# Kernel optimization log

Hardware: AMD Instinct MI355X
Metric: run time of the kernel (lower is better)

The kernel has to match this reference:

```python
import jax, jax.numpy as jnp
import numpy as np
import math

N, D, E, M, MODS = 16384, 1024, 5, 64, 5
K = 1  # top-k for sparse router


def setup_inputs() -> dict:
    key = jax.random.key(0)
    ks = jax.random.split(key, 24)
    rn = lambda k, shape, s=1.0: jax.random.normal(k, shape, dtype=jnp.float32) * s
    inp = {
        'x': rn(ks[0], (N, D)),
        'spectrogram': rn(ks[1], (N, D)),
        'waveform': rn(ks[2], (N, D)),
        'pitch': rn(ks[3], (N, D)),
        'envelope': rn(ks[4], (N, D)),
        'phase': rn(ks[5], (N, D)),
        # routers (torch Linear: y = x @ W.T + b, W is [out,in]); init std=0.01
        'Wsoft': rn(ks[6], (E, D), 0.01), 'bsoft': jnp.zeros((E,), jnp.float32),
        'Wsparse': rn(ks[7], (E, D), 0.01), 'bsparse': jnp.zeros((E,), jnp.float32),
        # memory (plain randn, not re-initialized)
        'm_key': rn(ks[8], (M, D)), 'm_val': rn(ks[9], (M, E)),
        # experts: Linear(D,D) -> SiLU -> Linear(D,D), stacked over E
        'W1': rn(ks[10], (E, D, D), 0.01), 'b1': jnp.zeros((E, D), jnp.float32),
        'W2': rn(ks[11], (E, D, D), 0.01), 'b2': jnp.zeros((E, D), jnp.float32),
        # fusion gates: Linear(D,1) + sigmoid, one per modality
        'Wg': rn(ks[12], (MODS, D), 0.01), 'bg': jnp.zeros((MODS,), jnp.float32),
        # fusion projection: Linear(D*MODS, D)
        'Wf': rn(ks[13], (D, D * MODS), 0.01), 'bf': jnp.zeros((D,), jnp.float32),
    }
    return inp


def reference(x, spectrogram, waveform, pitch, envelope, phase,
              Wsoft, bsoft, Wsparse, bsparse, m_key, m_val,
              W1, b1, W2, b2, Wg, bg, Wf, bf):
    alpha_moe = jnp.float32(0.5)
    alpha_fusion = jnp.float32(0.5)

    # soft router: softmax(Linear)
    soft_w = jax.nn.softmax(x @ Wsoft.T + bsoft, axis=-1)          # [N,E]

    # sparse router: top-k + softmax, scattered back to [N,E]
    logits = x @ Wsparse.T + bsparse                               # [N,E]
    top_vals, top_idx = jax.lax.top_k(logits, K)                   # [N,K]
    sparse_gates = jax.nn.softmax(top_vals, axis=-1)               # [N,K]
    one_hot = jax.nn.one_hot(top_idx, E, dtype=logits.dtype)       # [N,K,E]
    sparse_w = jnp.sum(one_hot * sparse_gates[..., None], axis=1)  # [N,E]

    # memory-augmented gating
    attn = jax.nn.softmax((x @ m_key.T) / math.sqrt(D), axis=-1)   # [N,M]
    memory_w = jax.nn.softmax(attn @ m_val, axis=-1)               # [N,E]

    mixed_w = alpha_moe * sparse_w + (1 - alpha_moe) * soft_w
    final_w = (mixed_w + memory_w) / 2                             # [N,E]

    # dense all-expert MLP: [N,E,D]
    h = jax.nn.silu(jnp.einsum('nd,eod->neo', x, W1) + b1)
    expert_out = jnp.einsum('ned,eod->neo', h, W2) + b2
    moe_output = jnp.einsum('neo,ne->no', expert_out, final_w)     # [N,D]

    # gated multimodal fusion
    features = [spectrogram, waveform, pitch, envelope, phase]
    gates = jax.nn.sigmoid(x @ Wg.T + bg)                          # [N,MODS]
    scaled = [gates[:, q:q + 1] * features[q] for q in range(MODS)]
    fused = jnp.concatenate(scaled, axis=-1) @ Wf.T + bf           # [N,D]

    return alpha_fusion * fused + (1 - alpha_fusion) * moe_output
```

## Files before the change

### kernel.cpp

```cpp
#include <hip/hip_runtime.h>
#include <stdint.h>

typedef __bf16 bf16x8 __attribute__((ext_vector_type(8)));
typedef float f32x4 __attribute__((ext_vector_type(4)));
typedef unsigned short u16;
typedef u16 ushort8 __attribute__((ext_vector_type(8)));
typedef u16 ushort4v __attribute__((ext_vector_type(4)));

__device__ __forceinline__ u16 f2bf(float f) {
    uint32_t u = __builtin_bit_cast(uint32_t, f);
    u += 0x7FFFu + ((u >> 16) & 1u);
    return (u16)(u >> 16);
}

__device__ __forceinline__ void gload16(const void* g, void* l) {
    __builtin_amdgcn_global_load_lds(
        reinterpret_cast<const __attribute__((address_space(1))) void*>(reinterpret_cast<uintptr_t>(g)),
        reinterpret_cast<__attribute__((address_space(3))) void*>(reinterpret_cast<uintptr_t>(l)),
        16, 0, 0);
}

#define BAR() asm volatile("s_barrier" ::: "memory")

template <int MODE>
__global__ __launch_bounds__(512, 2)
void gemm256(const u16* __restrict__ A, int lda,
             const u16* __restrict__ B, int ldb, int K,
             void* __restrict__ Cout, int ldc,
             const float* __restrict__ bias, const float* __restrict__ fw05)
{
    __shared__ __align__(16) u16 As[2 * 256 * 64];
    __shared__ __align__(16) u16 Bs[2 * 256 * 64];

    const int t    = threadIdx.x;
    const int lane = t & 63;
    const int wave = t >> 6;
    const int l16  = lane & 15;
    const int lhi  = lane >> 4;
    const int wm   = wave >> 2;
    const int wn   = wave & 3;

    const int gx  = gridDim.x;
    const int nwg = gx * gridDim.y;
    int id  = blockIdx.y * gx + blockIdx.x;
    int swz = (nwg & 7) ? id : ((id & 7) * (nwg >> 3) + (id >> 3));
    const int bx = swz % gx;
    const int by = swz / gx;

    const size_t rowBase = (size_t)by * 256;
    const int    colBase = bx * 256;
    const int    NT      = K >> 6;

    const int rl0 = t >> 3;
    const int ko0 = (t & 7) * 8;
    const int kos = ((t & 7) ^ (rl0 & 7)) * 8;

    const u16* aRow = A + (rowBase + rl0) * (size_t)lda + kos;
    const u16* bRow = B + (size_t)(colBase + rl0) * ldb + kos;
    u16* asW = As + rl0 * 64 + ko0;
    u16* bsW = Bs + rl0 * 64 + ko0;

#define STA(bufo, e, r0, r1)                                                     \
    do {                                                                         \
        gload16(aRow + (size_t)(r0) * lda + (e), asW + (bufo) + (r0) * 64);      \
        gload16(aRow + (size_t)(r1) * lda + (e), asW + (bufo) + (r1) * 64);      \
    } while (0)
#define STB(bufo, e, b0)                                                         \
    do {                                                                         \
        gload16(bRow + (size_t)(b0) * ldb + (e), bsW + (bufo) + (b0) * 64);      \
        gload16(bRow + (size_t)((b0) + 64) * ldb + (e),                          \
                bsW + (bufo) + ((b0) + 64) * 64);                                \
    } while (0)

    const int sw = l16 & 7;
    const u16* aRd0 = As + (wm * 128 + l16) * 64 + ((lhi ^ sw) * 8);
    const u16* aRd1 = As + (wm * 128 + l16) * 64 + (((lhi + 4) ^ sw) * 8);
    const u16* bRd0 = Bs + (wn * 64 + l16) * 64 + ((lhi ^ sw) * 8);
    const u16* bRd1 = Bs + (wn * 64 + l16) * 64 + (((lhi + 4) ^ sw) * 8);

    f32x4 acc[8][4];
#pragma unroll
    for (int i = 0; i < 8; i++)
#pragma unroll
        for (int j = 0; j < 4; j++)
            acc[i][j] = (f32x4){0.f, 0.f, 0.f, 0.f};

    STA(0, 0, 0, 128);
    STA(0, 0, 64, 192);
    STB(0, 0, 0);
    STB(0, 0, 128);
    const int e1p = (NT > 1) ? 64 : 0;
    STB(16384, e1p, 0);
    STB(16384, e1p, 128);
    STA(16384, e1p, 0, 128);
    asm volatile("s_waitcnt vmcnt(6)" ::: "memory");
    BAR();

    bf16x8 bfr[4][2];
    for (int tt = 0; tt < NT; ++tt) {
        const int c  = (tt & 1) << 14;
        const int cn = c ^ 16384;
        const int e1 = ((tt + 1 < NT) ? tt + 1 : NT - 1) << 6;
        const int e2 = ((tt + 2 < NT) ? tt + 2 : NT - 1) << 6;

#pragma unroll
        for (int q = 0; q < 4; ++q) {
            bf16x8 af[2][2];
#pragma unroll
            for (int s = 0; s < 2; ++s) {
                af[s][0] = *(const bf16x8*)(aRd0 + c + (2 * q + s) * 16 * 64);
                af[s][1] = *(const bf16x8*)(aRd1 + c + (2 * q + s) * 16 * 64);
            }
            if (q == 0) {
#pragma unroll
                for (int ni = 0; ni < 4; ++ni) {
                    bfr[ni][0] = *(const bf16x8*)(bRd0 + c + ni * 16 * 64);
                    bfr[ni][1] = *(const bf16x8*)(bRd1 + c + ni * 16 * 64);
                }
                STA(cn, e1, 64, 192);
            } else if (q == 1) {
                STB(c, e2, 0);
            } else if (q == 2) {
                STB(c, e2, 128);
            } else {
                STA(c, e2, 0, 128);
            }
            BAR();
            __builtin_amdgcn_s_setprio(1);
#pragma unroll
            for (int s = 0; s < 2; ++s)
#pragma unroll
                for (int ni = 0; ni < 4; ++ni)
#pragma unroll
                    for (int kk = 0; kk < 2; ++kk)
                        acc[2 * q + s][ni] = __builtin_amdgcn_mfma_f32_16x16x32_bf16(
                            af[s][kk], bfr[ni][kk], acc[2 * q + s][ni], 0, 0, 0);
            __builtin_amdgcn_s_setprio(0);
            if (q == 3) asm volatile("s_waitcnt vmcnt(6)" ::: "memory");
            BAR();
        }
    }

    const int orow = wm * 128 + lhi * 4;
    const int ocol = colBase + wn * 64 + l16;

    if constexpr (MODE == 0) {
        u16* C = (u16*)Cout;
        const int eidx = colBase >> 10;
#pragma unroll
        for (int mi = 0; mi < 8; mi++) {
#pragma unroll
            for (int j = 0; j < 4; j++) {
                size_t r = rowBase + orow + mi * 16 + j;
                float w = fw05[r * 5 + eidx];
#pragma unroll
                for (int ni = 0; ni < 4; ni++) {
                    int cc = ocol + ni * 16;
                    float v = acc[mi][ni][j] + bias[cc];
                    float s = v / (1.f + __expf(-v));
                    C[r * (size_t)ldc + cc] = f2bf(w * s);
                }
            }
        }
    } else {
        float* C = (float*)Cout;
#pragma unroll
        for (int mi = 0; mi < 8; mi++) {
#pragma unroll
            for (int j = 0; j < 4; j++) {
                size_t r = rowBase + orow + mi * 16 + j;
#pragma unroll
                for (int ni = 0; ni < 4; ni++) {
                    size_t idx = r * (size_t)ldc + (ocol + ni * 16);
                    C[idx] = acc[mi][ni][j];
                }
            }
        }
    }
#undef STA
#undef STB
}

__global__ __launch_bounds__(256)
void router_kernel(const float* __restrict__ x,
                   const float* __restrict__ Wsoft, const float* __restrict__ Wsparse,
                   const float* __restrict__ m_key, const float* __restrict__ Wg,
                   float* __restrict__ logits, u16* __restrict__ Xbf)
{
    __shared__ float Xs[128][66];
    __shared__ float Ws[80][132];

    const int t    = threadIdx.x;
    const int lane = t & 63;
    const int wave = t >> 6;
    const int row0 = blockIdx.x * 64;

    float acc[20];
#pragma unroll
    for (int c = 0; c < 20; c++) acc[c] = 0.f;

    for (int k0 = 0; k0 < 1024; k0 += 128) {
#pragma unroll
        for (int i = 0; i < 8; i++) {
            int f4 = i * 256 + t;
            int r  = f4 >> 5;
            int kk = (f4 & 31) * 4;
            f32x4 v = *(const f32x4*)(x + (size_t)(row0 + r) * 1024 + k0 + kk);
            Xs[kk + 0][r] = v[0]; Xs[kk + 1][r] = v[1];
            Xs[kk + 2][r] = v[2]; Xs[kk + 3][r] = v[3];
            ushort4v o4;
            o4[0] = f2bf(v[0]); o4[1] = f2bf(v[1]);
            o4[2] = f2bf(v[2]); o4[3] = f2bf(v[3]);
            *(ushort4v*)(Xbf + (size_t)(row0 + r) * 1024 + k0 + kk) = o4;
        }
#pragma unroll
        for (int i = 0; i < 10; i++) {
            int f4 = i * 256 + t;
            int j  = f4 >> 5;
            int kk = (f4 & 31) * 4;
            const float* src;
            if      (j < 5)  src = Wsoft   + (size_t)j * 1024;
            else if (j < 10) src = Wsparse + (size_t)(j - 5) * 1024;
            else if (j < 74) src = m_key   + (size_t)(j - 10) * 1024;
            else             src = Wg      + (size_t)(j - 74) * 1024;
            *(f32x4*)&Ws[j][kk] = *(const f32x4*)(src + k0 + kk);
        }
        __syncthreads();

        for (int k4 = 0; k4 < 32; k4++) {
            float x0 = Xs[k4 * 4 + 0][lane];
            float x1 = Xs[k4 * 4 + 1][lane];
            float x2 = Xs[k4 * 4 + 2][lane];
            float x3 = Xs[k4 * 4 + 3][lane];
#pragma unroll
            for (int c = 0; c < 20; c++) {
                f32x4 w = *(const f32x4*)&Ws[wave * 20 + c][k4 * 4];
                acc[c] += x0 * w[0] + x1 * w[1] + x2 * w[2] + x3 * w[3];
            }
        }
        __syncthreads();
    }

    float* dst = logits + (size_t)(row0 + lane) * 80 + wave * 20;
#pragma unroll
    for (int c = 0; c < 20; c++) dst[c] = acc[c];
}

__global__ __launch_bounds__(256)
void finalize_kernel(const float* __restrict__ logits, const float* __restrict__ m_val,
                     const float* __restrict__ bsoft, const float* __restrict__ bsparse,
                     const float* __restrict__ bg,
                     float* __restrict__ fw05, float* __restrict__ g05,
                     u16* __restrict__ Abuf, int NC)
{
    __shared__ float mv[320];
    for (int i = threadIdx.x; i < 320; i += 256) mv[i] = m_val[i];
    __syncthreads();

    int idx = blockIdx.x * 256 + threadIdx.x;
    if (idx >= NC) return;
    const float* L = logits + (size_t)idx * 80;

    float sl[5];
#pragma unroll
    for (int e = 0; e < 5; e++) sl[e] = L[e] + bsoft[e];
    float sm = sl[0];
#pragma unroll
    for (int e = 1; e < 5; e++) sm = fmaxf(sm, sl[e]);
    float ssum = 0.f, sw[5];
#pragma unroll
    for (int e = 0; e < 5; e++) { sw[e] = __expf(sl[e] - sm); ssum += sw[e]; }
    float sinv = 1.f / ssum;

    int am = 0; float bv = L[5] + bsparse[0];
#pragma unroll
    for (int e = 1; e < 5; e++) {
        float v = L[5 + e] + bsparse[e];
        if (v > bv) { bv = v; am = e; }
    }

    float amax = -1e30f;
    for (int m = 0; m < 64; m++) amax = fmaxf(amax, L[10 + m] * 0.03125f);
    float asum = 0.f, mw[5] = {0.f, 0.f, 0.f, 0.f, 0.f};
    for (int m = 0; m < 64; m++) {
        float a = __expf(L[10 + m] * 0.03125f - amax);
        asum += a;
#pragma unroll
        for (int e = 0; e < 5; e++) mw[e] += a * mv[m * 5 + e];
    }
    float ainv = 1.f / asum;
#pragma unroll
    for (int e = 0; e < 5; e++) mw[e] *= ainv;
    float mm = mw[0];
#pragma unroll
    for (int e = 1; e < 5; e++) mm = fmaxf(mm, mw[e]);
    float msum = 0.f, me[5];
#pragma unroll
    for (int e = 0; e < 5; e++) { me[e] = __expf(mw[e] - mm); msum += me[e]; }
    float minv = 1.f / msum;

    u16* ta = Abuf + (size_t)idx * 10368;
#pragma unroll
    for (int e = 0; e < 5; e++) {
        float fv = 0.125f * ((e == am) ? 1.f : 0.f) + 0.125f * sw[e] * sinv
                 + 0.25f * me[e] * minv;
        fw05[(size_t)idx * 5 + e] = fv;
        ta[5120 + e] = f2bf(fv);
    }
#pragma unroll
    for (int q = 0; q < 5; q++)
        g05[(size_t)idx * 5 + q] = 0.5f / (1.f + __expf(-(L[74 + q] + bg[q])));

    for (int j = 5125; j < 5184; j++) ta[j] = 0;
    ta[10304] = f2bf(0.5f);
    for (int j = 10305; j < 10368; j++) ta[j] = 0;
}

__global__ __launch_bounds__(256)
void cast_bf16_kernel(const float* __restrict__ src, u16* __restrict__ dst, size_t n)
{
    size_t i = ((size_t)blockIdx.x * 256 + threadIdx.x) * 8;
    if (i >= n) return;
    f32x4 a = *(const f32x4*)(src + i);
    f32x4 b = *(const f32x4*)(src + i + 4);
    ushort8 o;
    o[0] = f2bf(a[0]); o[1] = f2bf(a[1]); o[2] = f2bf(a[2]); o[3] = f2bf(a[3]);
    o[4] = f2bf(b[0]); o[5] = f2bf(b[1]); o[6] = f2bf(b[2]); o[7] = f2bf(b[3]);
    *(ushort8*)(dst + i) = o;
}

__global__ __launch_bounds__(256)
void prep_wcat(const float* __restrict__ W2, const float* __restrict__ b2,
               const float* __restrict__ Wf, const float* __restrict__ bfias,
               u16* __restrict__ out)
{
    size_t tid = (size_t)blockIdx.x * 256 + threadIdx.x;
    int o  = (int)(tid / 1296);
    int c0 = (int)(tid % 1296) * 8;
    ushort8 v;
    if (c0 + 8 <= 5120) {
        int e = c0 >> 10, d = c0 & 1023;
        const float* s = W2 + ((size_t)e * 1024 + o) * 1024 + d;
        f32x4 a = *(const f32x4*)s;
        f32x4 b = *(const f32x4*)(s + 4);
        v[0] = f2bf(a[0]); v[1] = f2bf(a[1]); v[2] = f2bf(a[2]); v[3] = f2bf(a[3]);
        v[4] = f2bf(b[0]); v[5] = f2bf(b[1]); v[6] = f2bf(b[2]); v[7] = f2bf(b[3]);
    } else if (c0 < 5184) {
#pragma unroll
        for (int jj = 0; jj < 8; jj++) {
            int c = c0 + jj;
            float f = (c >= 5120 && c < 5125) ? b2[(size_t)(c - 5120) * 1024 + o] : 0.f;
            v[jj] = f2bf(f);
        }
    } else {
        int c2 = c0 - 5184;
        if (c2 + 8 <= 5120) {
            const float* s = Wf + (size_t)o * 5120 + c2;
            f32x4 a = *(const f32x4*)s;
            f32x4 b = *(const f32x4*)(s + 4);
            v[0] = f2bf(a[0]); v[1] = f2bf(a[1]); v[2] = f2bf(a[2]); v[3] = f2bf(a[3]);
            v[4] = f2bf(b[0]); v[5] = f2bf(b[1]); v[6] = f2bf(b[2]); v[7] = f2bf(b[3]);
        } else {
#pragma unroll
            for (int jj = 0; jj < 8; jj++) {
                int cj = c2 + jj;
                v[jj] = f2bf((cj == 5120) ? bfias[o] : 0.f);
            }
        }
    }
    *(ushort8*)(out + (size_t)o * 10368 + c0) = v;
}

__global__ __launch_bounds__(256)
void build_afused(const float* __restrict__ f0, const float* __restrict__ f1,
                  const float* __restrict__ f2, const float* __restrict__ f3,
                  const float* __restrict__ f4,
                  const float* __restrict__ g05, u16* __restrict__ Abuf)
{
    size_t tid = (size_t)blockIdx.x * 256 + threadIdx.x;
    size_t r  = tid / 640;
    int   c0  = (int)(tid % 640) * 8;
    int   q   = c0 >> 10;
    int   d   = c0 & 1023;
    const float* fq = (q == 0) ? f0 : (q == 1) ? f1 : (q == 2) ? f2 : (q == 3) ? f3 : f4;
    float g = g05[r * 5 + q];
    f32x4 a = *(const f32x4*)(fq + r * 1024 + d);
    f32x4 b = *(const f32x4*)(fq + r * 1024 + d + 4);
    ushort8 v;
    v[0] = f2bf(g * a[0]); v[1] = f2bf(g * a[1]); v[2] = f2bf(g * a[2]); v[3] = f2bf(g * a[3]);
    v[4] = f2bf(g * b[0]); v[5] = f2bf(g * b[1]); v[6] = f2bf(g * b[2]); v[7] = f2bf(g * b[3]);
    *(ushort8*)(Abuf + r * 10368 + 5184 + c0) = v;
}

extern "C" void kernel_launch(void* const* d_in, const int* in_sizes, int n_in,
                              void* d_out, int out_size, void* d_ws, size_t ws_size,
                              hipStream_t stream)
{
    (void)in_sizes; (void)n_in; (void)out_size;

    const float* x      = (const float*)d_in[0];
    const float* spect  = (const float*)d_in[1];
    const float* wavef  = (const float*)d_in[2];
    const float* pitch  = (const float*)d_in[3];
    const float* envel  = (const float*)d_in[4];
    const float* phase  = (const float*)d_in[5];
    const float* Wsoft  = (const float*)d_in[6];
    const float* bsoft  = (const float*)d_in[7];
    const float* Wsparse= (const float*)d_in[8];
    const float* bsparse= (const float*)d_in[9];
    const float* m_key  = (const float*)d_in[10];
    const float* m_val  = (const float*)d_in[11];
    const float* W1     = (const float*)d_in[12];
    const float* b1     = (const float*)d_in[13];
    const float* W2     = (const float*)d_in[14];
    const float* b2     = (const float*)d_in[15];
    const float* Wg     = (const float*)d_in[16];
    const float* bg     = (const float*)d_in[17];
    const float* Wf     = (const float*)d_in[18];
    const float* bfias  = (const float*)d_in[19];
    float* out = (float*)d_out;

    const int N = 16384;

    size_t fixed = (size_t)5 * 1024 * 1024 * 2 + (size_t)1024 * 10368 * 2;
    int NC = 16384;
    while (NC > 256 && fixed + (size_t)NC * 23144 > ws_size) NC >>= 1;

    char* p = (char*)d_ws;
    u16* W1bf = (u16*)p; p += (size_t)5 * 1024 * 1024 * 2;
    u16* Wcat = (u16*)p; p += (size_t)1024 * 10368 * 2;
    u16* Xbf  = (u16*)p; p += (size_t)NC * 1024 * 2;
    u16* Abuf = (u16*)p; p += (size_t)NC * 10368 * 2;
    float* logits = (float*)p; p += (size_t)NC * 80 * 4;
    float* fw05   = (float*)p; p += (size_t)NC * 5 * 4;
    float* g05    = (float*)p; p += (size_t)NC * 5 * 4;

    cast_bf16_kernel<<<2560, 256, 0, stream>>>(W1, W1bf, (size_t)5 * 1024 * 1024);
    prep_wcat<<<5184, 256, 0, stream>>>(W2, b2, Wf, bfias, Wcat);

    for (int n0 = 0; n0 < N; n0 += NC) {
        const size_t off = (size_t)n0 * 1024;

        router_kernel<<<NC / 64, 256, 0, stream>>>(x + off, Wsoft, Wsparse, m_key, Wg,
                                                   logits, Xbf);
        finalize_kernel<<<(NC + 255) / 256, 256, 0, stream>>>(
            logits, m_val, bsoft, bsparse, bg, fw05, g05, Abuf, NC);

        build_afused<<<(unsigned)((size_t)NC * 640 / 256), 256, 0, stream>>>(
            spect + off, wavef + off, pitch + off, envel + off, phase + off,
            g05, Abuf);

        gemm256<0><<<dim3(20, NC / 256), 512, 0, stream>>>(
            Xbf, 1024, W1bf, 1024, 1024, Abuf, 10368, b1, fw05);

        gemm256<1><<<dim3(4, NC / 256), 512, 0, stream>>>(
            Abuf, 10368, Wcat, 10368, 10368, out + off, 1024, nullptr, nullptr);
    }
}
```

Measured before the change: 709.8 us.

## Fuse five expert column tiles into one persistent block reusing the X tile

Replaces the first-layer expert GEMM launch with a dedicated kernel in which each block walks five 256-column segments, one per expert, in a single pipelined 80-step K loop. After every 16 steps it applies bias, SiLU and the per-row gate weight, writes bf16 output and zeroes the accumulators. The aim is to cut block count and re-fetches of the same A rows, which should stay in cache, and to keep the pipeline primed across segments. In exchange the grid shrinks from 20 to 4 column blocks, which lowers parallelism, and the epilogue now stalls the main loop inline.

```diff
diff --git a/kernel.cpp b/kernel.cpp
--- a/kernel.cpp
+++ b/kernel.cpp
@@ -21,6 +21,7 @@
 }
 
 #define BAR() asm volatile("s_barrier" ::: "memory")
+
 
 template <int MODE>
 __global__ __launch_bounds__(512, 2)
@@ -144,41 +145,169 @@
     const int orow = wm * 128 + lhi * 4;
     const int ocol = colBase + wn * 64 + l16;
 
-    if constexpr (MODE == 0) {
-        u16* C = (u16*)Cout;
-        const int eidx = colBase >> 10;
-#pragma unroll
-        for (int mi = 0; mi < 8; mi++) {
-#pragma unroll
-            for (int j = 0; j < 4; j++) {
-                size_t r = rowBase + orow + mi * 16 + j;
-                float w = fw05[r * 5 + eidx];
-#pragma unroll
-                for (int ni = 0; ni < 4; ni++) {
-                    int cc = ocol + ni * 16;
-                    float v = acc[mi][ni][j] + bias[cc];
-                    float s = v / (1.f + __expf(-v));
-                    C[r * (size_t)ldc + cc] = f2bf(w * s);
-                }
-            }
-        }
-    } else {
-        float* C = (float*)Cout;
-#pragma unroll
-        for (int mi = 0; mi < 8; mi++) {
-#pragma unroll
-            for (int j = 0; j < 4; j++) {
-                size_t r = rowBase + orow + mi * 16 + j;
-#pragma unroll
-                for (int ni = 0; ni < 4; ni++) {
-                    size_t idx = r * (size_t)ldc + (ocol + ni * 16);
-                    C[idx] = acc[mi][ni][j];
-                }
+    float* C = (float*)Cout;
+#pragma unroll
+    for (int mi = 0; mi < 8; mi++) {
+#pragma unroll
+        for (int j = 0; j < 4; j++) {
+            size_t r = rowBase + orow + mi * 16 + j;
+#pragma unroll
+            for (int ni = 0; ni < 4; ni++) {
+                size_t idx = r * (size_t)ldc + (ocol + ni * 16);
+                C[idx] = acc[mi][ni][j];
             }
         }
     }
 #undef STA
 #undef STB
+}
+
+__global__ __launch_bounds__(512, 2)
+void gemm_moe(const u16* __restrict__ A, const u16* __restrict__ B,
+              u16* __restrict__ C, const float* __restrict__ bias,
+              const float* __restrict__ fw05)
+{
+    __shared__ __align__(16) u16 As[2 * 256 * 64];
+    __shared__ __align__(16) u16 Bs[2 * 256 * 64];
+
+    const int t    = threadIdx.x;
+    const int lane = t & 63;
+    const int wave = t >> 6;
+    const int l16  = lane & 15;
+    const int lhi  = lane >> 4;
+    const int wm   = wave >> 2;
+    const int wn   = wave & 3;
+
+    const int gx  = gridDim.x;
+    const int nwg = gx * gridDim.y;
+    int id  = blockIdx.y * gx + blockIdx.x;
+    int swz = (nwg & 7) ? id : ((id & 7) * (nwg >> 3) + (id >> 3));
+    const int bx = swz % gx;
+    const int by = swz / gx;
+    const size_t rowBase = (size_t)by * 256;
+
+    const int rl0 = t >> 3;
+    const int ko0 = (t & 7) * 8;
+    const int kos = ((t & 7) ^ (rl0 & 7)) * 8;
+
+    const u16* aRow = A + (rowBase + rl0) * (size_t)1024 + kos;
+    const u16* bThr = B + (size_t)rl0 * 1024 + kos;
+    u16* asW = As + rl0 * 64 + ko0;
+    u16* bsW = Bs + rl0 * 64 + ko0;
+
+#define COLOFF(s) ((size_t)(bx + 4 * (s)) << 18)
+#define STA(bufo, e, r0, r1)                                                     \
+    do {                                                                         \
+        gload16(aRow + (size_t)(r0) * 1024 + (e), asW + (bufo) + (r0) * 64);     \
+        gload16(aRow + (size_t)(r1) * 1024 + (e), asW + (bufo) + (r1) * 64);     \
+    } while (0)
+#define STB2(bp, bufo, e, b0)                                                    \
+    do {                                                                         \
+        gload16((bp) + (size_t)(b0) * 1024 + (e), bsW + (bufo) + (b0) * 64);     \
+        gload16((bp) + (size_t)((b0) + 64) * 1024 + (e),                         \
+                bsW + (bufo) + ((b0) + 64) * 64);                                \
+    } while (0)
+
+    const int sw = l16 & 7;
+    const u16* aRd0 = As + (wm * 128 + l16) * 64 + ((lhi ^ sw) * 8);
+    const u16* aRd1 = As + (wm * 128 + l16) * 64 + (((lhi + 4) ^ sw) * 8);
+    const u16* bRd0 = Bs + (wn * 64 + l16) * 64 + ((lhi ^ sw) * 8);
+    const u16* bRd1 = Bs + (wn * 64 + l16) * 64 + (((lhi + 4) ^ sw) * 8);
+
+    f32x4 acc[8][4];
+#pragma unroll
+    for (int i = 0; i < 8; i++)
+#pragma unroll
+        for (int j = 0; j < 4; j++)
+            acc[i][j] = (f32x4){0.f, 0.f, 0.f, 0.f};
+
+    {
+        const u16* bR0 = bThr + COLOFF(0);
+        STA(0, 0, 0, 128);
+        STA(0, 0, 64, 192);
+        STB2(bR0, 0, 0, 0);
+        STB2(bR0, 0, 0, 128);
+        STB2(bR0, 16384, 64, 0);
+        STB2(bR0, 16384, 64, 128);
+        STA(16384, 64, 0, 128);
+    }
+    asm volatile("s_waitcnt vmcnt(6)" ::: "memory");
+    BAR();
+
+    const int orow = wm * 128 + lhi * 4;
+
+    bf16x8 bfr[4][2];
+    for (int v = 0; v < 80; ++v) {
+        const int c  = (v & 1) << 14;
+        const int cn = c ^ 16384;
+        const int v1 = (v + 1 < 80) ? v + 1 : 79;
+        const int v2 = (v + 2 < 80) ? v + 2 : 79;
+        const int e1 = (v1 & 15) << 6;
+        const int e2 = (v2 & 15) << 6;
+        const u16* bR2 = bThr + COLOFF(v2 >> 4);
+
+#pragma unroll
+        for (int q = 0; q < 4; ++q) {
+            bf16x8 af[2][2];
+#pragma unroll
+            for (int s = 0; s < 2; ++s) {
+                af[s][0] = *(const bf16x8*)(aRd0 + c + (2 * q + s) * 16 * 64);
+                af[s][1] = *(const bf16x8*)(aRd1 + c + (2 * q + s) * 16 * 64);
+            }
+            if (q == 0) {
+#pragma unroll
+                for (int ni = 0; ni < 4; ++ni) {
+                    bfr[ni][0] = *(const bf16x8*)(bRd0 + c + ni * 16 * 64);
+                    bfr[ni][1] = *(const bf16x8*)(bRd1 + c + ni * 16 * 64);
+                }
+                STA(cn, e1, 64, 192);
+            } else if (q == 1) {
+                STB2(bR2, c, e2, 0);
+            } else if (q == 2) {
+                STB2(bR2, c, e2, 128);
+            } else {
+                STA(c, e2, 0, 128);
+            }
+            BAR();
+            __builtin_amdgcn_s_setprio(1);
+#pragma unroll
+            for (int s = 0; s < 2; ++s)
+#pragma unroll
+                for (int ni = 0; ni < 4; ++ni)
+#pragma unroll
+                    for (int kk = 0; kk < 2; ++kk)
+                        acc[2 * q + s][ni] = __builtin_amdgcn_mfma_f32_16x16x32_bf16(
+                            af[s][kk], bfr[ni][kk], acc[2 * q + s][ni], 0, 0, 0);
+            __builtin_amdgcn_s_setprio(0);
+            if (q == 3) asm volatile("s_waitcnt vmcnt(6)" ::: "memory");
+            BAR();
+        }
+
+        if ((v & 15) == 15) {
+            const int seg     = v >> 4;
+            const int colBase = (bx + 4 * seg) * 256;
+            const int ocol    = colBase + wn * 64 + l16;
+#pragma unroll
+            for (int mi = 0; mi < 8; mi++) {
+#pragma unroll
+                for (int j = 0; j < 4; j++) {
+                    size_t r = rowBase + orow + mi * 16 + j;
+                    float w = fw05[r * 5 + seg];
+#pragma unroll
+                    for (int ni = 0; ni < 4; ni++) {
+                        int cc = ocol + ni * 16;
+                        float vv = acc[mi][ni][j] + bias[cc];
+                        float sl = vv / (1.f + __expf(-vv));
+                        C[r * (size_t)10368 + cc] = f2bf(w * sl);
+                        acc[mi][ni][j] = 0.f;
+                    }
+                }
+            }
+        }
+    }
+#undef STA
+#undef STB2
+#undef COLOFF
 }
 
 __global__ __launch_bounds__(256)
@@ -450,8 +579,7 @@
             spect + off, wavef + off, pitch + off, envel + off, phase + off,
             g05, Abuf);
 
-        gemm256<0><<<dim3(20, NC / 256), 512, 0, stream>>>(
-            Xbf, 1024, W1bf, 1024, 1024, Abuf, 10368, b1, fw05);
+        gemm_moe<<<dim3(4, NC / 256), 512, 0, stream>>>(Xbf, W1bf, Abuf, b1, fw05);
 
         gemm256<1><<<dim3(4, NC / 256), 512, 0, stream>>>(
             Abuf, 10368, Wcat, 10368, 10368, out + off, 1024, nullptr, nullptr);
```

Measured after the change: 746.6 us. 1.05x slower.
